# Performance work log

Hardware: AMD Instinct MI355X
Metric: run time of the kernel (lower is better)

## Reference

```python
import jax, jax.numpy as jnp
import numpy as np

STRIDES = [8, 16, 32, 64, 128]
CELL_ANCHORS = np.array([
 [[-18.0,-8.0,25.0,15.0],[-23.7183,-11.1191,30.7183,18.1191],[-30.9228,-15.0488,37.9228,22.0488],[-12.0,-12.0,19.0,19.0],[-16.1587,-16.1587,23.1587,23.1587],[-21.3984,-21.3984,28.3984,28.3984],[-8.0,-20.0,15.0,27.0],[-11.1191,-26.2381,18.1191,33.2381],[-15.0488,-34.0976,22.0488,41.0976]],
 [[-38.0,-16.0,53.0,31.0],[-49.9564,-22.2381,64.9564,37.2381],[-65.0204,-30.0976,80.0204,45.0976],[-24.0,-24.0,39.0,39.0],[-32.3175,-32.3175,47.3175,47.3175],[-42.7968,-42.7968,57.7968,57.7968],[-14.0,-36.0,29.0,51.0],[-19.7183,-47.4365,34.7183,62.4365],[-26.9228,-61.8456,41.9228,76.8456]],
 [[-74.0,-28.0,105.0,59.0],[-97.3929,-39.4365,128.3929,70.4365],[-126.8661,-53.8456,157.8661,84.8456],[-48.0,-48.0,79.0,79.0],[-64.6349,-64.6349,95.6349,95.6349],[-85.5937,-85.5937,116.5937,116.5937],[-30.0,-76.0,61.0,107.0],[-41.9564,-99.9127,72.9564,130.9127],[-57.0204,-130.0409,88.0204,161.0409]],
 [[-150.0,-60.0,213.0,123.0],[-197.3056,-83.9127,260.3056,146.9127],[-256.907,-114.0409,319.907,177.0409],[-96.0,-96.0,159.0,159.0],[-129.2699,-129.2699,192.2699,192.2699],[-171.1873,-171.1873,234.1873,234.1873],[-58.0,-148.0,121.0,211.0],[-81.3929,-194.7858,144.3929,257.7858],[-110.8661,-253.7322,173.8661,316.7322]],
 [[-298.0,-116.0,425.0,243.0],[-392.0914,-162.7858,519.0914,289.7858],[-510.6392,-221.7322,637.6392,348.7322],[-192.0,-192.0,319.0,319.0],[-258.5398,-258.5398,385.5398,385.5398],[-342.3747,-342.3747,469.3747,469.3747],[-118.0,-300.0,245.0,427.0],[-165.3056,-394.6113,292.3056,521.6113],[-224.907,-513.814,351.907,640.814]]], dtype=np.float32)
THRESHOLD = 0.05
TOP_N = 1000
NMS_THR = 0.5
DETECTIONS = 100


def conv3x3(x, w, b):
    y = jax.lax.conv_general_dilated(x, w, (1, 1), ((1, 1), (1, 1)),
                                     dimension_numbers=('NCHW', 'OIHW', 'NCHW'))
    return y + b[None, :, None, None]


def run_head(x, ws, bs):
    for w, b in zip(ws[:-1], bs[:-1]):
        x = jax.nn.relu(conv3x3(x, w, b))
    return conv3x3(x, ws[-1], bs[-1])


def delta2box(deltas, anchors, w, h, stride):
    awh = anchors[:, 2:] - anchors[:, :2] + 1.0
    ctr = anchors[:, :2] + 0.5 * awh
    pctr = deltas[:, :2] * awh + ctr
    pwh = jnp.exp(deltas[:, 2:]) * awh
    M = jnp.array([w * stride - 1.0, h * stride - 1.0], dtype=deltas.dtype)
    clamp = lambda t: jnp.clip(t, 0.0, M)
    return jnp.concatenate([clamp(pctr - 0.5 * pwh), clamp(pctr + 0.5 * pwh - 1.0)], axis=1)


def decode_level(cls_map, box_map, stride, anchors):
    # cls_map: (B, A*C, H, W) post-sigmoid; box_map: (B, A*4, H, W)
    B, AC, H, W = cls_map.shape
    A = anchors.shape[0]
    C = AC // A

    def one(cm, bm):
        flat = cm.reshape(-1)                      # (A*C*H*W,)
        scores, idx = jax.lax.top_k(flat, TOP_N)
        cls = (idx // (W * H)) % C
        x = idx % W
        y = (idx // W) % H
        a = idx // (C * H * W)
        deltas = bm.reshape(A, 4, H, W)[a, :, y, x]      # (TOP_N, 4)
        grid = jnp.stack([x, y, x, y], axis=1).astype(flat.dtype) * stride + anchors[a]
        boxes = delta2box(deltas, grid, W, H, stride)
        valid = scores >= THRESHOLD                # emulates threshold filter + zero padding
        return (jnp.where(valid, scores, 0.0),
                jnp.where(valid[:, None], boxes, 0.0),
                jnp.where(valid, cls.astype(flat.dtype), 0.0))

    return jax.vmap(one)(cls_map, box_map)


def nms_all(scores, boxes, classes):
    # per-class greedy NMS, fixed DETECTIONS output slots
    def one(s, b, c):
        order = jnp.argsort(-s)
        s, b, c = s[order], b[order], c[order]
        areas = (b[:, 2] - b[:, 0] + 1.0) * (b[:, 3] - b[:, 1] + 1.0)
        state = (s > 0,
                 jnp.zeros((DETECTIONS,), s.dtype),
                 jnp.zeros((DETECTIONS, 4), s.dtype),
                 jnp.zeros((DETECTIONS,), s.dtype))

        def body(i, st):
            valid, os_, ob_, oc_ = st
            any_v = jnp.any(valid)
            idx = jnp.argmax(valid)                # first remaining box (highest score)
            bi, si, ci, ai = b[idx], s[idx], c[idx], areas[idx]
            xy1 = jnp.maximum(b[:, :2], bi[:2])
            xy2 = jnp.minimum(b[:, 2:], bi[2:])
            inter = jnp.prod(jnp.clip(xy2 - xy1 + 1.0, 0.0, None), axis=1)
            iou = inter / (areas + ai - inter)
            suppress = (s <= si) & (iou > NMS_THR) & (c == ci)
            valid = valid & jnp.where(any_v, ~suppress, True)
            os_ = os_.at[i].set(jnp.where(any_v, si, 0.0))
            ob_ = ob_.at[i].set(jnp.where(any_v, bi, jnp.zeros_like(bi)))
            oc_ = oc_.at[i].set(jnp.where(any_v, ci, 0.0))
            return (valid, os_, ob_, oc_)

        _, os_, ob_, oc_ = jax.lax.fori_loop(0, DETECTIONS, body, state)
        return os_, ob_, oc_

    return jax.vmap(one)(scores, boxes, classes)


def _forward(feats, cls_ws, cls_bs, box_ws, box_bs):
    cls_heads = [jax.nn.sigmoid(run_head(f, cls_ws, cls_bs)) for f in feats]
    box_heads = [run_head(f, box_ws, box_bs) for f in feats]
    parts = [decode_level(ch, bh, STRIDES[i], jnp.asarray(CELL_ANCHORS[i]))
             for i, (ch, bh) in enumerate(zip(cls_heads, box_heads))]
    scores = jnp.concatenate([p[0] for p in parts], axis=1)
    boxes = jnp.concatenate([p[1] for p in parts], axis=1)
    classes = jnp.concatenate([p[2] for p in parts], axis=1)
    return nms_all(scores, boxes, classes)


def setup_inputs() -> dict:
    key = jax.random.key(0)
    ks = jax.random.split(key, 32)
    B = 2
    sizes = [64, 32, 16, 8, 4]
    inp = {}
    for i, s in enumerate(sizes):
        inp['feat%d' % i] = jax.random.normal(ks[i], (B, 256, s, s), jnp.float32)
    cls_out = [256, 256, 256, 256, 720]
    box_out = [256, 256, 256, 256, 36]
    for i in range(5):
        inp['cls_w%d' % i] = jax.random.normal(ks[5 + i], (cls_out[i], 256, 3, 3), jnp.float32) * 0.01
        inp['cls_b%d' % i] = jnp.zeros((cls_out[i],), jnp.float32)
        inp['box_w%d' % i] = jax.random.normal(ks[15 + i], (box_out[i], 256, 3, 3), jnp.float32) * 0.01
        inp['box_b%d' % i] = jnp.zeros((box_out[i],), jnp.float32)
    return inp


def reference(feat0, feat1, feat2, feat3, feat4,
              cls_w0, cls_w1, cls_w2, cls_w3, cls_w4,
              cls_b0, cls_b1, cls_b2, cls_b3, cls_b4,
              box_w0, box_w1, box_w2, box_w3, box_w4,
              box_b0, box_b1, box_b2, box_b3, box_b4):
    feats = [feat0, feat1, feat2, feat3, feat4]
    cls_ws = [cls_w0, cls_w1, cls_w2, cls_w3, cls_w4]
    cls_bs = [cls_b0, cls_b1, cls_b2, cls_b3, cls_b4]
    box_ws = [box_w0, box_w1, box_w2, box_w3, box_w4]
    box_bs = [box_b0, box_b1, box_b2, box_b3, box_b4]
    return _forward(feats, cls_ws, cls_bs, box_ws, box_bs)
```

## Files before the change

### kernel.cpp

```cpp
#include <hip/hip_runtime.h>
#include <math.h>

typedef unsigned long long U64;
#define CCAP 4096

__constant__ float cANCH[180] = {
  -18.0f,-8.0f,25.0f,15.0f, -23.7183f,-11.1191f,30.7183f,18.1191f, -30.9228f,-15.0488f,37.9228f,22.0488f,
  -12.0f,-12.0f,19.0f,19.0f, -16.1587f,-16.1587f,23.1587f,23.1587f, -21.3984f,-21.3984f,28.3984f,28.3984f,
  -8.0f,-20.0f,15.0f,27.0f, -11.1191f,-26.2381f,18.1191f,33.2381f, -15.0488f,-34.0976f,22.0488f,41.0976f,
  -38.0f,-16.0f,53.0f,31.0f, -49.9564f,-22.2381f,64.9564f,37.2381f, -65.0204f,-30.0976f,80.0204f,45.0976f,
  -24.0f,-24.0f,39.0f,39.0f, -32.3175f,-32.3175f,47.3175f,47.3175f, -42.7968f,-42.7968f,57.7968f,57.7968f,
  -14.0f,-36.0f,29.0f,51.0f, -19.7183f,-47.4365f,34.7183f,62.4365f, -26.9228f,-61.8456f,41.9228f,76.8456f,
  -74.0f,-28.0f,105.0f,59.0f, -97.3929f,-39.4365f,128.3929f,70.4365f, -126.8661f,-53.8456f,157.8661f,84.8456f,
  -48.0f,-48.0f,79.0f,79.0f, -64.6349f,-64.6349f,95.6349f,95.6349f, -85.5937f,-85.5937f,116.5937f,116.5937f,
  -30.0f,-76.0f,61.0f,107.0f, -41.9564f,-99.9127f,72.9564f,130.9127f, -57.0204f,-130.0409f,88.0204f,161.0409f,
  -150.0f,-60.0f,213.0f,123.0f, -197.3056f,-83.9127f,260.3056f,146.9127f, -256.907f,-114.0409f,319.907f,177.0409f,
  -96.0f,-96.0f,159.0f,159.0f, -129.2699f,-129.2699f,192.2699f,192.2699f, -171.1873f,-171.1873f,234.1873f,234.1873f,
  -58.0f,-148.0f,121.0f,211.0f, -81.3929f,-194.7858f,144.3929f,257.7858f, -110.8661f,-253.7322f,173.8661f,316.7322f,
  -298.0f,-116.0f,425.0f,243.0f, -392.0914f,-162.7858f,519.0914f,289.7858f, -510.6392f,-221.7322f,637.6392f,348.7322f,
  -192.0f,-192.0f,319.0f,319.0f, -258.5398f,-258.5398f,385.5398f,385.5398f, -342.3747f,-342.3747f,469.3747f,469.3747f,
  -118.0f,-300.0f,245.0f,427.0f, -165.3056f,-394.6113f,292.3056f,521.6113f, -224.907f,-513.814f,351.907f,640.814f
};

__device__ __constant__ int dH[5]      = {64,32,16,8,4};
__device__ __constant__ int dLogW[5]   = {6,5,4,3,2};
__device__ __constant__ int dHW[5]     = {4096,1024,256,64,16};
__device__ __constant__ int dPW[5]     = {66,34,18,10,6};
__device__ __constant__ int dPS[5]     = {4356,1156,324,100,36};
__device__ __constant__ int dPadOff[5] = {0,2230272,2822144,2988032,3039232};
__device__ __constant__ int dCO[5]     = {0,5898240,7372800,7741440,7833600};
__device__ __constant__ int dBO[5]     = {0,294912,368640,387072,391680};
__device__ __constant__ float dStrF[5] = {8.f,16.f,32.f,64.f,128.f};
__device__ __constant__ int dBase[6]   = {0,32,40,42,44,46};
__device__ __constant__ int dNPB[5]    = {16,4,1,1,1};

__global__ void fill_zero4(float4* __restrict__ p, int n4) {
  for (int i = blockIdx.x*blockDim.x + threadIdx.x; i < n4; i += gridDim.x*blockDim.x)
    p[i] = make_float4(0.f,0.f,0.f,0.f);
}

__global__ void pad_one_p4(const float* __restrict__ f, float* __restrict__ P,
                           int n, int logHW, int logW, int W, int PW, int PS) {
  const int HW1 = (1<<logHW) - 1;
  for (int i = blockIdx.x*blockDim.x + threadIdx.x; i < n; i += gridDim.x*blockDim.x) {
    const int bc = i >> logHW;
    const int p  = i & HW1;
    const int b = bc >> 8, c = bc & 255;
    const int y = p >> logW, x = p & (W-1);
    const int vpix = (y+1)*PW + (x+1);
    P[(((size_t)(b*64 + (c>>2)))*PS + vpix)*4 + (c&3)] = f[i];
  }
}

__global__ void transp_w(const float* __restrict__ w, float* __restrict__ wT,
                         int Cout, int OCP) {
  const int n = 9*256*OCP;
  for (int i = blockIdx.x*blockDim.x + threadIdx.x; i < n; i += gridDim.x*blockDim.x) {
    const int oc = i % OCP;
    const int kt = i / OCP;
    const int k  = kt % 256;
    const int t  = kt / 256;
    wT[i] = (oc < Cout) ? w[(size_t)oc*2304 + k*9 + t] : 0.f;
  }
}

#define QUAD(KB, Q)                                                     \
  {                                                                     \
    const float* __restrict__ w0 = wp + (size_t)((KB)+0)*OCL;           \
    const float* __restrict__ w1 = wp + (size_t)((KB)+1)*OCL;           \
    const float* __restrict__ w2 = wp + (size_t)((KB)+2)*OCL;           \
    const float* __restrict__ w3 = wp + (size_t)((KB)+3)*OCL;           \
    _Pragma("unroll") for (int o=0;o<16;++o) acc[o]=fmaf(w0[o],(Q).x,acc[o]); \
    _Pragma("unroll") for (int o=0;o<16;++o) acc[o]=fmaf(w1[o],(Q).y,acc[o]); \
    _Pragma("unroll") for (int o=0;o<16;++o) acc[o]=fmaf(w2[o],(Q).z,acc[o]); \
    _Pragma("unroll") for (int o=0;o<16;++o) acc[o]=fmaf(w3[o],(Q).w,acc[o]); \
  }

__global__ __launch_bounds__(256)
void conv_hidden(const float* __restrict__ IN, float* __restrict__ OUT,
                 const float* __restrict__ wT, const float* __restrict__ bias)
{
  const int OCL = 256;
  const int bx = blockIdx.x;
  if (bx >= 46) return;
  int l = 0;
  if (bx >= dBase[1]) l = 1;
  if (bx >= dBase[2]) l = 2;
  if (bx >= dBase[3]) l = 3;
  if (bx >= dBase[4]) l = 4;
  const int npb = dNPB[l];
  const int rel = bx - dBase[l];
  const int b = rel / npb, pb = rel % npb;
  const int W = dH[l], logW = dLogW[l], HW = dHW[l], PW = dPW[l], PS = dPS[l];
  const int pix = pb*256 + threadIdx.x;
  if (pix >= HW) return;
  const int y = pix >> logW, x = pix & (W-1);
  const int voff = (y+1)*PW + (x+1);
  const float4* __restrict__ P4 = (const float4*)(IN + dPadOff[l]);
  const float4* __restrict__ inB = P4 + (size_t)b*64*PS + voff;
  const int oc0 = blockIdx.y * 16;
  float acc[16];
#pragma unroll
  for (int o = 0; o < 16; ++o) acc[o] = 0.f;
#pragma unroll 1
  for (int t = 0; t < 9; ++t) {
    const int dy = t / 3, dx = t - dy * 3;
    const float4* __restrict__ ip = inB + ((dy-1)*PW + (dx-1));
    const float* __restrict__ wp = wT + (size_t)t*256*OCL + oc0;
#pragma unroll 1
    for (int k0 = 0; k0 < 256; k0 += 16) {
      const int kq = k0 >> 2;
      const float4 q0 = ip[(size_t)(kq+0)*PS];
      const float4 q1 = ip[(size_t)(kq+1)*PS];
      const float4 q2 = ip[(size_t)(kq+2)*PS];
      const float4 q3 = ip[(size_t)(kq+3)*PS];
      QUAD(k0+ 0, q0);
      QUAD(k0+ 4, q1);
      QUAD(k0+ 8, q2);
      QUAD(k0+12, q3);
    }
  }
  float4* __restrict__ O4 = (float4*)(OUT + dPadOff[l]);
  float4* __restrict__ op = O4 + ((size_t)b*64 + (oc0 >> 2))*PS + voff;
#pragma unroll
  for (int j = 0; j < 4; ++j) {
    const float4 sv = make_float4(
      fmaxf(acc[4*j+0] + bias[oc0+4*j+0], 0.f),
      fmaxf(acc[4*j+1] + bias[oc0+4*j+1], 0.f),
      fmaxf(acc[4*j+2] + bias[oc0+4*j+2], 0.f),
      fmaxf(acc[4*j+3] + bias[oc0+4*j+3], 0.f));
    op[(size_t)j*PS] = sv;
  }
}

__global__ __launch_bounds__(256)
void conv_final(const float* __restrict__ IN, float* __restrict__ OUT,
                const float* __restrict__ wT, const float* __restrict__ bias,
                int Cout, int OCL, int isCls)
{
  const int bx = blockIdx.x;
  if (bx >= 46) return;
  int l = 0;
  if (bx >= dBase[1]) l = 1;
  if (bx >= dBase[2]) l = 2;
  if (bx >= dBase[3]) l = 3;
  if (bx >= dBase[4]) l = 4;
  const int npb = dNPB[l];
  const int rel = bx - dBase[l];
  const int b = rel / npb, pb = rel % npb;
  const int W = dH[l], logW = dLogW[l], HW = dHW[l], PW = dPW[l], PS = dPS[l];
  const int pix = pb*256 + threadIdx.x;
  if (pix >= HW) return;
  const int y = pix >> logW, x = pix & (W-1);
  const int voff = (y+1)*PW + (x+1);
  const float4* __restrict__ P4 = (const float4*)(IN + dPadOff[l]);
  const float4* __restrict__ inB = P4 + (size_t)b*64*PS + voff;
  const int oc0 = blockIdx.y * 16;
  float acc[16];
#pragma unroll
  for (int o = 0; o < 16; ++o) acc[o] = 0.f;
#pragma unroll 1
  for (int t = 0; t < 9; ++t) {
    const int dy = t / 3, dx = t - dy * 3;
    const float4* __restrict__ ip = inB + ((dy-1)*PW + (dx-1));
    const float* __restrict__ wp = wT + (size_t)t*256*OCL + oc0;
#pragma unroll 1
    for (int k0 = 0; k0 < 256; k0 += 16) {
      const int kq = k0 >> 2;
      const float4 q0 = ip[(size_t)(kq+0)*PS];
      const float4 q1 = ip[(size_t)(kq+1)*PS];
      const float4 q2 = ip[(size_t)(kq+2)*PS];
      const float4 q3 = ip[(size_t)(kq+3)*PS];
      QUAD(k0+ 0, q0);
      QUAD(k0+ 4, q1);
      QUAD(k0+ 8, q2);
      QUAD(k0+12, q3);
    }
  }
  const int outOff = isCls ? dCO[l] : dBO[l];
#pragma unroll
  for (int o = 0; o < 16; ++o) {
    const int oc = oc0 + o;
    if (oc < Cout) {
      float tv = acc[o] + bias[oc];
      if (isCls) tv = 1.f / (1.f + expf(-tv));
      OUT[(size_t)outOff + ((size_t)b*Cout + oc)*HW + pix] = tv;
    }
  }
}

__global__ void topk_init(unsigned* __restrict__ hist, unsigned* __restrict__ state) {
  for (int i = threadIdx.x; i < 2560; i += blockDim.x) hist[i] = 0u;
  if (threadIdx.x < 10) {
    state[threadIdx.x*4+0] = 0u; state[threadIdx.x*4+1] = 1000u;
    state[threadIdx.x*4+2] = 0u; state[threadIdx.x*4+3] = 0u;
  }
}

__global__ void topk_hist(const float* __restrict__ clsm, unsigned* __restrict__ hist,
                          const unsigned* __restrict__ state, int pass)
{
  __shared__ unsigned lh[256];
  const int id = blockIdx.y, l = id % 5, b = id / 5;
  const int N = 720 * dHW[l];
  const float* __restrict__ sp = clsm + dCO[l] + (size_t)b*720*dHW[l];
  for (int i = threadIdx.x; i < 256; i += blockDim.x) lh[i] = 0u;
  __syncthreads();
  const unsigned prefix = state[id*4];
  for (int i = blockIdx.x*blockDim.x + threadIdx.x; i < N; i += gridDim.x*blockDim.x) {
    const unsigned bits = __float_as_uint(sp[i]);
    unsigned bin; bool ok;
    if (pass == 0)      { bin = bits >> 24;          ok = true; }
    else if (pass == 1) { bin = (bits >> 16) & 0xFF; ok = ((bits >> 24) == prefix); }
    else                { bin = (bits >>  8) & 0xFF; ok = ((bits >> 16) == prefix); }
    if (ok) atomicAdd(&lh[bin], 1u);
  }
  __syncthreads();
  for (int i = threadIdx.x; i < 256; i += blockDim.x)
    if (lh[i]) atomicAdd(&hist[id*256 + i], lh[i]);
}

__global__ void topk_scan(unsigned* __restrict__ hist, unsigned* __restrict__ state) {
  const int id = threadIdx.x;
  if (id < 10) {
    const unsigned k = state[id*4+1];
    unsigned cum = 0; int d = 255;
    for (; d > 0; --d) {
      const unsigned h = hist[id*256 + d];
      if (cum + h >= k) break;
      cum += h;
    }
    state[id*4+0] = (state[id*4+0] << 8) | (unsigned)d;
    state[id*4+1] = k - cum;
  }
  __syncthreads();
  for (int i = threadIdx.x; i < 2560; i += blockDim.x) hist[i] = 0u;
}

__global__ void topk_compact(const float* __restrict__ clsm, unsigned* __restrict__ state,
                             U64* __restrict__ cbuf)
{
  const int id = blockIdx.y, l = id % 5, b = id / 5;
  const int N = 720 * dHW[l];
  const float* __restrict__ sp = clsm + dCO[l] + (size_t)b*720*dHW[l];
  const unsigned p24 = state[id*4];
  for (int i = blockIdx.x*blockDim.x + threadIdx.x; i < N; i += gridDim.x*blockDim.x) {
    const unsigned bits = __float_as_uint(sp[i]);
    if ((bits >> 8) >= p24) {
      const unsigned pos = atomicAdd(&state[id*4+2], 1u);
      if (pos < CCAP)
        cbuf[(size_t)id*CCAP + pos] = ((U64)bits << 32) | (U64)(0xFFFFFFFFu - (unsigned)i);
    }
  }
}

__global__ __launch_bounds__(1024)
void topk_sort_store(const U64* __restrict__ cbuf, const unsigned* __restrict__ state,
                     float* __restrict__ cand_s, float* __restrict__ cand_c,
                     unsigned* __restrict__ sel)
{
  __shared__ U64 sk[CCAP];
  const int id = blockIdx.x, l = id % 5, b = id / 5;
  const int t = threadIdx.x;
  unsigned M = state[id*4+2]; if (M > (unsigned)CCAP) M = CCAP;
  for (int i = t; i < CCAP; i += 1024) sk[i] = (i < (int)M) ? cbuf[(size_t)id*CCAP + i] : 0ull;
  __syncthreads();
  for (int k = 2; k <= CCAP; k <<= 1)
    for (int j = k >> 1; j > 0; j >>= 1) {
      for (int u = t; u < CCAP/2; u += 1024) {
        const int i1 = ((u & ~(j-1)) << 1) | (u & (j-1));
        const int i2 = i1 + j;
        const bool asc = ((i1 & k) == 0);
        const U64 a = sk[i1], c = sk[i2];
        if ((a < c) == asc) { sk[i1] = c; sk[i2] = a; }
      }
      __syncthreads();
    }
  const int HW = dHW[l];
  for (int j = t; j < 1000; j += 1024) {
    float sc_ = 0.f, cf = 0.f; unsigned sidx = 0xFFFFFFFFu;
    if (j < (int)M) {
      const U64 key = sk[j];
      const float s = __uint_as_float((unsigned)(key >> 32));
      const unsigned idx = 0xFFFFFFFFu - (unsigned)key;
      if (s >= 0.05f) {
        const int ch = (int)(idx / (unsigned)HW);
        const int cls = ch % 80;
        sc_ = s; cf = (float)cls; sidx = idx;
      }
    }
    const int slot = b*5000 + l*1000 + j;
    cand_s[slot] = sc_; cand_c[slot] = cf; sel[slot] = sidx;
  }
}

__global__ __launch_bounds__(1024)
void box_decode(const float* __restrict__ boxm, const float* __restrict__ cand_s,
                const unsigned* __restrict__ sel, float4* __restrict__ cand_b)
{
  const int id = blockIdx.x, l = id % 5, b = id / 5;
  const int HW = dHW[l], W = dH[l], logW = dLogW[l];
  const float stride = dStrF[l];
  const int j = threadIdx.x;
  if (j >= 1000) return;
  const int slot = b*5000 + l*1000 + j;
  float4 bx = make_float4(0.f,0.f,0.f,0.f);
  if (cand_s[slot] > 0.f) {
    const unsigned idx = sel[slot];
    const int pix = (int)(idx & (unsigned)(HW-1));
    const int ch  = (int)(idx >> (2*logW));
    const int a   = ch / 80;
    const int xx = pix & (W-1), yy = pix >> logW;
    const float* __restrict__ bm = boxm + dBO[l] + (size_t)b*36*HW;
    const float d0 = bm[(size_t)(a*4+0)*HW + pix];
    const float d1 = bm[(size_t)(a*4+1)*HW + pix];
    const float d2 = bm[(size_t)(a*4+2)*HW + pix];
    const float d3 = bm[(size_t)(a*4+3)*HW + pix];
    const float* A = &cANCH[l*36 + a*4];
    const float g0 = (float)xx * stride + A[0];
    const float g1 = (float)yy * stride + A[1];
    const float g2 = (float)xx * stride + A[2];
    const float g3 = (float)yy * stride + A[3];
    const float awx = g2 - g0 + 1.f, awy = g3 - g1 + 1.f;
    const float cx = g0 + 0.5f*awx, cy = g1 + 0.5f*awy;
    const float pcx = d0*awx + cx, pcy = d1*awy + cy;
    const float pwx = expf(d2)*awx, pwy = expf(d3)*awy;
    const float Mx = (float)W*stride - 1.f, My = (float)W*stride - 1.f;
    const float x1 = fminf(fmaxf(pcx - 0.5f*pwx, 0.f), Mx);
    const float y1 = fminf(fmaxf(pcy - 0.5f*pwy, 0.f), My);
    const float x2 = fminf(fmaxf(pcx + 0.5f*pwx - 1.f, 0.f), Mx);
    const float y2 = fminf(fmaxf(pcy + 0.5f*pwy - 1.f, 0.f), My);
    bx = make_float4(x1, y1, x2, y2);
  }
  cand_b[slot] = bx;
}

__global__ __launch_bounds__(1024)
void nms_sort(const float* __restrict__ cs, const float4* __restrict__ cb, const float* __restrict__ cc,
              float* __restrict__ ss, float4* __restrict__ sb, float* __restrict__ sc)
{
  extern __shared__ U64 sk[];
  const int b = blockIdx.x;
  const int t = threadIdx.x;
  for (int i = t; i < 8192; i += 1024) {
    U64 key = 0ull;
    if (i < 5000) {
      const unsigned bits = __float_as_uint(cs[b*5000 + i]);
      key = ((U64)bits << 32) | (U64)(0xFFFFFFFFu - (unsigned)i);
    }
    sk[i] = key;
  }
  __syncthreads();
  for (int k = 2; k <= 8192; k <<= 1)
    for (int j = k >> 1; j > 0; j >>= 1) {
      for (int u = t; u < 4096; u += 1024) {
        const int i1 = ((u & ~(j-1)) << 1) | (u & (j-1));
        const int i2 = i1 + j;
        const bool asc = ((i1 & k) == 0);
        const U64 a = sk[i1], c = sk[i2];
        if ((a < c) == asc) { sk[i1] = c; sk[i2] = a; }
      }
      __syncthreads();
    }
  for (int i = t; i < 5000; i += 1024) {
    const unsigned pos = 0xFFFFFFFFu - (unsigned)sk[i];
    ss[b*5008 + i] = cs[b*5000 + pos];
    sb[b*5008 + i] = cb[b*5000 + pos];
    sc[b*5008 + i] = cc[b*5000 + pos];
  }
}

__global__ __launch_bounds__(1024)
void nms_greedy(const float* __restrict__ ss, const float4* __restrict__ sb, const float* __restrict__ sc,
                float* __restrict__ outp)
{
  const int b = blockIdx.x;
  const int t = threadIdx.x;
  __shared__ int red[16];
  __shared__ int selSh;
  __shared__ float bc[8];

  const float* SS = ss + (size_t)b*5008;
  const float4* SB = sb + (size_t)b*5008;
  const float* SC = sc + (size_t)b*5008;

  float s[5], c[5], ar[5]; float4 bx[5]; bool val[5];
#pragma unroll
  for (int k = 0; k < 5; ++k) {
    const int j = t + k*1024;
    if (j < 5000) {
      s[k] = SS[j]; c[k] = SC[j]; bx[k] = SB[j];
      val[k] = (s[k] > 0.f);
      ar[k] = (bx[k].z - bx[k].x + 1.f) * (bx[k].w - bx[k].y + 1.f);
    } else {
      s[k] = 0.f; c[k] = 0.f; bx[k] = make_float4(0.f,0.f,0.f,0.f);
      val[k] = false; ar[k] = 1.f;
    }
  }

  for (int i = 0; i < 100; ++i) {
    int loc = 0x7FFFFFFF;
#pragma unroll
    for (int k = 0; k < 5; ++k) if (val[k]) { const int j = t + k*1024; loc = (j < loc) ? j : loc; }
    for (int off = 32; off > 0; off >>= 1) { const int o = __shfl_down(loc, off); loc = (o < loc) ? o : loc; }
    if ((t & 63) == 0) red[t >> 6] = loc;
    __syncthreads();
    if (t < 64) {
      int v = (t < 16) ? red[t] : 0x7FFFFFFF;
      for (int off = 8; off > 0; off >>= 1) { const int o = __shfl_down(v, off); v = (o < v) ? o : v; }
      if (t == 0) selSh = v;
    }
    __syncthreads();
    const int sel_ = selSh;
    if (sel_ == 0x7FFFFFFF) {
      if (t == 0) {
        outp[b*100 + i] = 0.f;
        outp[200 + (b*100 + i)*4 + 0] = 0.f;
        outp[200 + (b*100 + i)*4 + 1] = 0.f;
        outp[200 + (b*100 + i)*4 + 2] = 0.f;
        outp[200 + (b*100 + i)*4 + 3] = 0.f;
        outp[1000 + b*100 + i] = 0.f;
      }
    } else {
      if (t == (sel_ & 1023)) {
        const int k = sel_ >> 10;
        bc[0] = s[k]; bc[1] = c[k];
        bc[2] = bx[k].x; bc[3] = bx[k].y; bc[4] = bx[k].z; bc[5] = bx[k].w;
        bc[6] = ar[k];
        outp[b*100 + i] = s[k];
        outp[200 + (b*100 + i)*4 + 0] = bx[k].x;
        outp[200 + (b*100 + i)*4 + 1] = bx[k].y;
        outp[200 + (b*100 + i)*4 + 2] = bx[k].z;
        outp[200 + (b*100 + i)*4 + 3] = bx[k].w;
        outp[1000 + b*100 + i] = c[k];
      }
      __syncthreads();
      const float si = bc[0], ci = bc[1], ai = bc[6];
      const float bix = bc[2], biy = bc[3], biz = bc[4], biw = bc[5];
#pragma unroll
      for (int k = 0; k < 5; ++k) {
        if (!val[k]) continue;
        const float xx1 = fmaxf(bx[k].x, bix), yy1 = fmaxf(bx[k].y, biy);
        const float xx2 = fminf(bx[k].z, biz), yy2 = fminf(bx[k].w, biw);
        const float iw = fmaxf(xx2 - xx1 + 1.f, 0.f), ih = fmaxf(yy2 - yy1 + 1.f, 0.f);
        const float inter = iw * ih;
        const float iou = inter / (ar[k] + ai - inter);
        if (s[k] <= si && iou > 0.5f && c[k] == ci) val[k] = false;
      }
    }
    __syncthreads();
  }
}

extern "C" void kernel_launch(void* const* d_in, const int* in_sizes, int n_in,
                              void* d_out, int out_size, void* d_ws, size_t ws_size,
                              hipStream_t stream)
{
  (void)in_sizes; (void)n_in; (void)out_size; (void)ws_size;
  const float* feat[5]; const float* cwp[5]; const float* cbp[5]; const float* bwp[5]; const float* bbp[5];
  for (int i = 0; i < 5; ++i) feat[i] = (const float*)d_in[i];
  for (int i = 0; i < 5; ++i) {
    cwp[i] = (const float*)d_in[5 + 4*i + 0];
    cbp[i] = (const float*)d_in[5 + 4*i + 1];
    bwp[i] = (const float*)d_in[5 + 4*i + 2];
    bbp[i] = (const float*)d_in[5 + 4*i + 3];
  }

  float* ws = (float*)d_ws;
  const size_t BUFSZ = 3057664;
  float* P     = ws;
  float* A     = ws + BUFSZ;
  float* Bb    = ws + 2*BUFSZ;
  float* clsm  = ws + 3*BUFSZ;
  float* boxm  = clsm + 7856640;
  float* wT    = boxm + 392832;
  float* cand_s = wT + 1769472;
  float* cand_b = cand_s + 10000;
  float* cand_c = cand_b + 40000;
  float* srt_s  = cand_c + 10000;
  float* srt_b  = srt_s + 10016;
  float* srt_c  = srt_b + 40064;
  unsigned* sel   = (unsigned*)(srt_c + 10016);
  unsigned* hist  = (unsigned*)(srt_c + 20016);
  unsigned* state = (unsigned*)(srt_c + 22576);
  U64*      cbuf  = (U64*)(srt_c + 22616);

  const int hHW[5]    = {4096,1024,256,64,16};
  const int hLogHW[5] = {12,10,8,6,4};
  const int hLogW[5]  = {6,5,4,3,2};
  const int hW[5]     = {64,32,16,8,4};
  const int hPW[5]    = {66,34,18,10,6};
  const int hPS[5]    = {4356,1156,324,100,36};
  const int hPadOff[5]= {0,2230272,2822144,2988032,3039232};

  fill_zero4<<<2048, 256, 0, stream>>>((float4*)P, (int)(3*BUFSZ/4));

  for (int l = 0; l < 5; ++l) {
    const int n = 2*256*hHW[l];
    int g = (n + 255)/256; if (g > 2048) g = 2048;
    pad_one_p4<<<g, 256, 0, stream>>>(feat[l], P + hPadOff[l], n, hLogHW[l], hLogW[l],
                                      hW[l], hPW[l], hPS[l]);
  }

  auto runHidden = [&](const float* w, const float* bias, const float* src, float* dst) {
    transp_w<<<2304, 256, 0, stream>>>(w, wT, 256, 256);
    conv_hidden<<<dim3(48, 16), dim3(256), 0, stream>>>(src, dst, wT, bias);
  };

  runHidden(cwp[0], cbp[0], P,  A);
  runHidden(cwp[1], cbp[1], A,  Bb);
  runHidden(cwp[2], cbp[2], Bb, A);
  runHidden(cwp[3], cbp[3], A,  Bb);
  transp_w<<<6480, 256, 0, stream>>>(cwp[4], wT, 720, 720);
  conv_final<<<dim3(48, 45), dim3(256), 0, stream>>>(Bb, clsm, wT, cbp[4], 720, 720, 1);

  topk_init<<<1, 1024, 0, stream>>>(hist, state);
  for (int pass = 0; pass < 3; ++pass) {
    topk_hist<<<dim3(128, 10), dim3(256), 0, stream>>>(clsm, hist, state, pass);
    topk_scan<<<1, 256, 0, stream>>>(hist, state);
  }
  topk_compact<<<dim3(128, 10), dim3(256), 0, stream>>>(clsm, state, cbuf);
  topk_sort_store<<<10, 1024, 0, stream>>>(cbuf, state, cand_s, cand_c, sel);

  runHidden(bwp[0], bbp[0], P,  A);
  runHidden(bwp[1], bbp[1], A,  Bb);
  runHidden(bwp[2], bbp[2], Bb, A);
  runHidden(bwp[3], bbp[3], A,  Bb);
  transp_w<<<432, 256, 0, stream>>>(bwp[4], wT, 36, 48);
  conv_final<<<dim3(48, 3), dim3(256), 0, stream>>>(Bb, boxm, wT, bbp[4], 36, 48, 0);

  box_decode<<<10, 1024, 0, stream>>>(boxm, cand_s, sel, (float4*)cand_b);

  nms_sort<<<dim3(2), dim3(1024), 8192*sizeof(U64), stream>>>(
      cand_s, (const float4*)cand_b, cand_c, srt_s, (float4*)srt_b, srt_c);
  nms_greedy<<<dim3(2), dim3(1024), 0, stream>>>(
      srt_s, (const float4*)srt_b, srt_c, (float*)d_out);
}
```

Measured before the change: 3.169 ms.

## Fuse classification and box head convolutions into shared batched launches

Runs the cls and box towers in the same kernel launch at each layer by doubling the grid's y dimension and picking the head per block. The aim is to fill the GPU better, since each conv launch had only 48x16 blocks, and to halve the number of sequential conv launches. It costs extra workspace for separate ping-pong buffers and weight regions per head, and a larger zero-fill.

```diff
diff --git a/kernel.cpp b/kernel.cpp
--- a/kernel.cpp
+++ b/kernel.cpp
@@ -77,8 +77,10 @@
   }
 
 __global__ __launch_bounds__(256)
-void conv_hidden(const float* __restrict__ IN, float* __restrict__ OUT,
-                 const float* __restrict__ wT, const float* __restrict__ bias)
+void conv_hidden_fused(const float* __restrict__ srcC, const float* __restrict__ srcB,
+                       float* __restrict__ dstC, float* __restrict__ dstB,
+                       const float* __restrict__ wTc, const float* __restrict__ wTb,
+                       const float* __restrict__ biasC, const float* __restrict__ biasB)
 {
   const int OCL = 256;
   const int bx = blockIdx.x;
@@ -94,11 +96,16 @@
   const int W = dH[l], logW = dLogW[l], HW = dHW[l], PW = dPW[l], PS = dPS[l];
   const int pix = pb*256 + threadIdx.x;
   if (pix >= HW) return;
+  const int head = blockIdx.y >> 4;
+  const float* __restrict__ IN  = head ? srcB : srcC;
+  float* __restrict__ OUT       = head ? dstB : dstC;
+  const float* __restrict__ wT  = head ? wTb : wTc;
+  const float* __restrict__ bias= head ? biasB : biasC;
   const int y = pix >> logW, x = pix & (W-1);
   const int voff = (y+1)*PW + (x+1);
   const float4* __restrict__ P4 = (const float4*)(IN + dPadOff[l]);
   const float4* __restrict__ inB = P4 + (size_t)b*64*PS + voff;
-  const int oc0 = blockIdx.y * 16;
+  const int oc0 = (blockIdx.y & 15) * 16;
   float acc[16];
 #pragma unroll
   for (int o = 0; o < 16; ++o) acc[o] = 0.f;
@@ -134,9 +141,10 @@
 }
 
 __global__ __launch_bounds__(256)
-void conv_final(const float* __restrict__ IN, float* __restrict__ OUT,
-                const float* __restrict__ wT, const float* __restrict__ bias,
-                int Cout, int OCL, int isCls)
+void conv_final_fused(const float* __restrict__ srcC, const float* __restrict__ srcB,
+                      float* __restrict__ clsm, float* __restrict__ boxm,
+                      const float* __restrict__ wTfc, const float* __restrict__ wTfb,
+                      const float* __restrict__ biasC, const float* __restrict__ biasB)
 {
   const int bx = blockIdx.x;
   if (bx >= 46) return;
@@ -151,11 +159,18 @@
   const int W = dH[l], logW = dLogW[l], HW = dHW[l], PW = dPW[l], PS = dPS[l];
   const int pix = pb*256 + threadIdx.x;
   if (pix >= HW) return;
+  const bool isCls = blockIdx.y < 45;
+  const int ocb = isCls ? blockIdx.y : (blockIdx.y - 45);
+  const int OCL = isCls ? 720 : 48;
+  const int Cout = isCls ? 720 : 36;
+  const float* __restrict__ IN  = isCls ? srcC : srcB;
+  const float* __restrict__ wT  = isCls ? wTfc : wTfb;
+  const float* __restrict__ bias= isCls ? biasC : biasB;
   const int y = pix >> logW, x = pix & (W-1);
   const int voff = (y+1)*PW + (x+1);
   const float4* __restrict__ P4 = (const float4*)(IN + dPadOff[l]);
   const float4* __restrict__ inB = P4 + (size_t)b*64*PS + voff;
-  const int oc0 = blockIdx.y * 16;
+  const int oc0 = ocb * 16;
   float acc[16];
 #pragma unroll
   for (int o = 0; o < 16; ++o) acc[o] = 0.f;
@@ -178,6 +193,7 @@
     }
   }
   const int outOff = isCls ? dCO[l] : dBO[l];
+  float* __restrict__ OUT = isCls ? clsm : boxm;
 #pragma unroll
   for (int o = 0; o < 16; ++o) {
     const int oc = oc0 + o;
@@ -469,12 +485,18 @@
   float* ws = (float*)d_ws;
   const size_t BUFSZ = 3057664;
   float* P     = ws;
-  float* A     = ws + BUFSZ;
-  float* Bb    = ws + 2*BUFSZ;
-  float* clsm  = ws + 3*BUFSZ;
+  float* Ac    = ws + BUFSZ;
+  float* Bc    = ws + 2*BUFSZ;
+  float* Ab    = ws + 3*BUFSZ;
+  float* Bb    = ws + 4*BUFSZ;
+  float* clsm  = ws + 5*BUFSZ;
   float* boxm  = clsm + 7856640;
-  float* wT    = boxm + 392832;
-  float* cand_s = wT + 1769472;
+  float* wreg  = boxm + 392832;
+  float* wTc   = wreg;
+  float* wTb   = wreg + 589824;
+  float* wTfc  = wreg;
+  float* wTfb  = wreg + 1658880;
+  float* cand_s = wreg + 1769472;
   float* cand_b = cand_s + 10000;
   float* cand_c = cand_b + 40000;
   float* srt_s  = cand_c + 10000;
@@ -493,7 +515,7 @@
   const int hPS[5]    = {4356,1156,324,100,36};
   const int hPadOff[5]= {0,2230272,2822144,2988032,3039232};
 
-  fill_zero4<<<2048, 256, 0, stream>>>((float4*)P, (int)(3*BUFSZ/4));
+  fill_zero4<<<2048, 256, 0, stream>>>((float4*)P, (int)(5*BUFSZ/4));
 
   for (int l = 0; l < 5; ++l) {
     const int n = 2*256*hHW[l];
@@ -502,17 +524,21 @@
                                       hW[l], hPW[l], hPS[l]);
   }
 
-  auto runHidden = [&](const float* w, const float* bias, const float* src, float* dst) {
-    transp_w<<<2304, 256, 0, stream>>>(w, wT, 256, 256);
-    conv_hidden<<<dim3(48, 16), dim3(256), 0, stream>>>(src, dst, wT, bias);
+  auto runFused = [&](int i, const float* sc_, const float* sb_, float* dc_, float* db_) {
+    transp_w<<<2304, 256, 0, stream>>>(cwp[i], wTc, 256, 256);
+    transp_w<<<2304, 256, 0, stream>>>(bwp[i], wTb, 256, 256);
+    conv_hidden_fused<<<dim3(48, 32), dim3(256), 0, stream>>>(
+        sc_, sb_, dc_, db_, wTc, wTb, cbp[i], bbp[i]);
   };
-
-  runHidden(cwp[0], cbp[0], P,  A);
-  runHidden(cwp[1], cbp[1], A,  Bb);
-  runHidden(cwp[2], cbp[2], Bb, A);
-  runHidden(cwp[3], cbp[3], A,  Bb);
-  transp_w<<<6480, 256, 0, stream>>>(cwp[4], wT, 720, 720);
-  conv_final<<<dim3(48, 45), dim3(256), 0, stream>>>(Bb, clsm, wT, cbp[4], 720, 720, 1);
+  runFused(0, P,  P,  Ac, Ab);
+  runFused(1, Ac, Ab, Bc, Bb);
+  runFused(2, Bc, Bb, Ac, Ab);
+  runFused(3, Ac, Ab, Bc, Bb);
+
+  transp_w<<<6480, 256, 0, stream>>>(cwp[4], wTfc, 720, 720);
+  transp_w<<<432, 256, 0, stream>>>(bwp[4], wTfb, 36, 48);
+  conv_final_fused<<<dim3(48, 48), dim3(256), 0, stream>>>(
+      Bc, Bb, clsm, boxm, wTfc, wTfb, cbp[4], bbp[4]);
 
   topk_init<<<1, 1024, 0, stream>>>(hist, state);
   for (int pass = 0; pass < 3; ++pass) {
@@ -522,13 +548,6 @@
   topk_compact<<<dim3(128, 10), dim3(256), 0, stream>>>(clsm, state, cbuf);
   topk_sort_store<<<10, 1024, 0, stream>>>(cbuf, state, cand_s, cand_c, sel);
 
-  runHidden(bwp[0], bbp[0], P,  A);
-  runHidden(bwp[1], bbp[1], A,  Bb);
-  runHidden(bwp[2], bbp[2], Bb, A);
-  runHidden(bwp[3], bbp[3], A,  Bb);
-  transp_w<<<432, 256, 0, stream>>>(bwp[4], wT, 36, 48);
-  conv_final<<<dim3(48, 3), dim3(256), 0, stream>>>(Bb, boxm, wT, bbp[4], 36, 48, 0);
-
   box_decode<<<10, 1024, 0, stream>>>(boxm, cand_s, sel, (float4*)cand_b);
 
   nms_sort<<<dim3(2), dim3(1024), 8192*sizeof(U64), stream>>>(
```

Result: faster. 2.941 ms (-7.2%).
